# Performance work log

Measured on AMD Instinct MI355X. Metric: run time of the kernel, lower is better.

The kernel has to match this reference:

```python
import jax, jax.numpy as jnp
import numpy as np

B, T, H = 256, 512, 512
NB = 2  # band_names = ['g', 'r']
D_IN = 1 + NB


def setup_inputs() -> dict:
    key = jax.random.key(0)
    ks = jax.random.split(key, 10)
    # serial band assignment: each valid timestep belongs to exactly one band
    band = jax.random.randint(ks[0], (B, T), 0, NB)
    valid = jax.random.uniform(ks[1], (B, T)) < 0.9
    s_onehot = (jax.nn.one_hot(band, NB) * valid[..., None].astype(jnp.float32)).astype(bool)
    onehot = valid
    dtime = jax.random.uniform(ks[2], (B, T))
    encz_last = jax.random.normal(ks[3], (B, H))
    scale = 1.0 / np.sqrt(H).astype(np.float32)
    W_ih = jax.random.normal(ks[4], (3 * H, D_IN)) * scale
    W_hh = jax.random.normal(ks[5], (3 * H, H)) * scale
    b_ih = jax.random.normal(ks[6], (3 * H,)) * scale
    b_hh = jax.random.normal(ks[7], (3 * H,)) * scale
    W1 = jax.random.normal(ks[8], (H, H)) * scale
    b1 = jnp.zeros((H,), jnp.float32)
    W2 = jax.random.normal(ks[9], (1, H)) * scale
    b2 = jnp.zeros((1,), jnp.float32)
    return dict(dtime=dtime, s_onehot=s_onehot, onehot=onehot, encz_last=encz_last,
                W_ih=W_ih, W_hh=W_hh, b_ih=b_ih, b_hh=b_hh, W1=W1, b1=b1, W2=W2, b2=b2)


def gru_masked(x, mask, h0, W_ih, W_hh, b_ih, b_hh):
    """Single-layer GRU (torch gate order r,z,n) with onehot mask: hidden held where mask==False."""
    xp = jnp.einsum('btd,gd->btg', x, W_ih) + b_ih  # [B,T,3H] precomputed input projections

    def step(h, inp):
        xg, m = inp  # xg [B,3H], m [B]
        hg = h @ W_hh.T + b_hh
        xr, xz, xn = jnp.split(xg, 3, axis=-1)
        hr, hz, hn = jnp.split(hg, 3, axis=-1)
        r = jax.nn.sigmoid(xr + hr)
        z = jax.nn.sigmoid(xz + hz)
        n = jnp.tanh(xn + r * hn)
        h_new = (1.0 - z) * n + z * h
        h_out = jnp.where(m[:, None], h_new, h)
        return h_out, h_out

    _, hs = jax.lax.scan(step, h0, (jnp.swapaxes(xp, 0, 1), jnp.swapaxes(mask, 0, 1)))
    return jnp.swapaxes(hs, 0, 1)  # [B,T,H]


def serial_to_parallel(x, m):
    """Compact serial entries where mask m is True to the front of the time axis; zeros elsewhere."""
    pos = jnp.cumsum(m.astype(jnp.int32), axis=1) - 1  # target slot per valid step
    pos = jnp.where(m, pos, 0)
    b_idx = jnp.arange(x.shape[0])[:, None]
    contrib = x * m[..., None].astype(x.dtype)
    return jnp.zeros_like(x).at[b_idx, pos].add(contrib)


def reference(dtime, s_onehot, onehot, encz_last, W_ih, W_hh, b_ih, b_hh, W1, b1, W2, b2):
    decz_in = jnp.concatenate([dtime[..., None], s_onehot.astype(dtime.dtype)], axis=-1)  # [B,T,3]
    decz = gru_masked(decz_in, onehot, encz_last, W_ih, W_hh, b_ih, b_hh)  # [B,T,H]
    hidden = jax.nn.relu(jnp.einsum('bth,oh->bto', decz, W1) + b1)
    decx = jnp.einsum('bth,oh->bto', hidden, W2) + b2  # [B,T,1]
    outs = [serial_to_parallel(decx, s_onehot[..., kb]) for kb in range(s_onehot.shape[-1])]
    return jnp.stack(outs, axis=0)  # [NB,B,T,1] -> model/decx.{b} per band
```

## Files before the change

kernel.cpp:

```cpp
#include <hip/hip_runtime.h>
#include <hip/hip_bf16.h>

#define BB 256
#define TT 512
#define HH 512

typedef float floatx4 __attribute__((ext_vector_type(4)));
typedef short short8 __attribute__((ext_vector_type(8)));

__device__ __forceinline__ unsigned short f2bf(float f) {
    union { float f; unsigned u; } v; v.f = f;
    unsigned r = v.u + 0x7fffu + ((v.u >> 16) & 1u);
    return (unsigned short)(r >> 16);
}
__device__ __forceinline__ float bf2f(unsigned short h) {
    union { unsigned u; float f; } v; v.u = ((unsigned)h) << 16;
    return v.f;
}
__device__ __forceinline__ int frag16(int b, int j) {
    int kin = j & 31;
    return (j >> 5) * 512 + (b + 16 * ((kin >> 2) & 3)) * 8 + ((kin >> 4) << 2) + (kin & 3);
}

__device__ __forceinline__ int ld_sc0(const int* p) {
    int v;
    asm volatile("global_load_dword %0, %1, off sc0\n\ts_waitcnt vmcnt(0)"
                 : "=v"(v) : "v"(p) : "memory");
    return v;
}

__global__ void detect_k(const unsigned char* __restrict__ s, int* __restrict__ flags)
{
    int a = 0, b = 0, c = 0;
    for (int i = blockIdx.x * blockDim.x + threadIdx.x; i < BB * TT * 2;
         i += gridDim.x * blockDim.x) {
        unsigned char v = s[i];
        if (v) {
            int m = i & 3;
            if (m == 1) a = 1;
            else if (m >= 2) b = 1;
            if ((i & 7) == 4) c = 1;
        }
    }
    if (a) atomicOr(flags, 1);
    if (b) atomicOr(flags, 2);
    if (c) atomicOr(flags, 4);
}

__global__ void canon_k(const void* __restrict__ s, const int* __restrict__ flags,
                        unsigned char* __restrict__ canon)
{
    int bt = blockIdx.x * blockDim.x + threadIdx.x;
    if (bt >= BB * TT) return;
    int f = *flags;
    int sg, sr;
    if (f & 1) {
        const unsigned char* p = (const unsigned char*)s;
        sg = p[2 * bt] != 0; sr = p[2 * bt + 1] != 0;
    } else if (f & 2) {
        const float* p = (const float*)s;
        sg = p[2 * bt] != 0.0f; sr = p[2 * bt + 1] != 0.0f;
    } else if (f & 4) {
        const int* p = (const int*)s;
        sg = p[2 * bt] != 0; sr = p[2 * bt + 1] != 0;
    } else {
        const long long* p = (const long long*)s;
        sg = p[2 * bt] != 0; sr = p[2 * bt + 1] != 0;
    }
    canon[bt] = (unsigned char)(sg | (sr << 1));
}

__global__ void h0_k(const float* __restrict__ encz, unsigned* __restrict__ Hp)
{
    int i = blockIdx.x * blockDim.x + threadIdx.x;
    if (i >= BB * HH / 2) return;
    int bg = i >> 8;
    int j  = (i & 255) * 2;
    float f0 = encz[bg * HH + j], f1 = encz[bg * HH + j + 1];
    unsigned short h0b = f2bf(f0), l0b = f2bf(f0 - bf2f(h0b));
    unsigned short h1b = f2bf(f1), l1b = f2bf(f1 - bf2f(h1b));
    int g = bg >> 4, b = bg & 15;
    int fi = frag16(b, j) >> 1;
    unsigned* base = Hp + (size_t)g * 32768;
    base[fi]        = (unsigned)h0b | ((unsigned)h1b << 16);
    base[4096 + fi] = (unsigned)l0b | ((unsigned)l1b << 16);
}

__global__ void w1h_k(const float* __restrict__ W1, unsigned short* __restrict__ W1h)
{
    int idx = blockIdx.x * blockDim.x + threadIdx.x;
    if (idx >= HH * HH) return;
    W1h[idx] = f2bf(W1[idx]);
}

template <bool FAST>
__device__ __forceinline__ void gru_loop(
    unsigned* Hbase, unsigned* hstage,
    const float* dtl, const unsigned char* cnl, float* exch, const float* pwl,
    unsigned short* decz, int* gcs, int* gcf,
    const short8* Bh, const short8* Bl,
    int tid, int w, int l, int wi, int bg0)
{
    int fastspin_en = 1;

    for (int t = 0; t < TT; ++t) {
        const char* src = (const char*)(Hbase + (size_t)(t & 3) * 8192);
        unsigned*   dst = Hbase + (size_t)((t + 1) & 3) * 8192;

        for (int c = w; c < 32; c += 6) {
            const void* gs = src + c * 1024 + l * 16;
            void* ls = (char*)hstage + c * 1024;
            __builtin_amdgcn_global_load_lds(
                (const __attribute__((address_space(1))) unsigned*)gs,
                (__attribute__((address_space(3))) unsigned*)ls, 16, 0,
                FAST ? 0x1 : 0x11);
        }
        __syncthreads();

        floatx4 ac0 = {0.f,0.f,0.f,0.f}, ac1 = {0.f,0.f,0.f,0.f}, ac2 = {0.f,0.f,0.f,0.f};
#pragma unroll
        for (int kt = 0; kt < 16; ++kt) {
            short8 ah = *(const short8*)((const char*)hstage + kt * 1024 + l * 16);
            short8 al = *(const short8*)((const char*)hstage + 16384 + kt * 1024 + l * 16);
            ac0 = __builtin_amdgcn_mfma_f32_16x16x32_bf16(ah, Bh[kt], ac0, 0, 0, 0);
            ac1 = __builtin_amdgcn_mfma_f32_16x16x32_bf16(ah, Bl[kt], ac1, 0, 0, 0);
            ac2 = __builtin_amdgcn_mfma_f32_16x16x32_bf16(al, Bh[kt], ac2, 0, 0, 0);
        }
        floatx4 acc = ac0 + ac1 + ac2;
        *(floatx4*)(exch + w * 256 + l * 4) = acc;
        __syncthreads();

        if (tid < 256) {
            const int b = tid >> 4;
            const int bgl = bg0 + b;
            const float dt = dtl[b * 516 + t];
            const unsigned char cn = cnl[b * 520 + t];
            const float sg = (cn & 1) ? 1.f : 0.f, sr = (cn & 2) ? 1.f : 0.f;
            const int jl0 = (tid * 2) & 31;
            const int j0  = wi * 32 + jl0;
            const int fi  = frag16(b, j0) >> 1;
            const unsigned hiw = hstage[fi];
            const unsigned low = hstage[4096 + fi];
            unsigned short hib[2], lob[2];
#pragma unroll
            for (int p = 0; p < 2; ++p) {
                int jl = jl0 + p;
                int lane16 = (jl & 15) + 16 * (b >> 2);
                int roff = b & 3;
                float a0 = exch[(jl >> 4) * 256 + lane16 * 4 + roff];
                float a1 = exch[(2 + (jl >> 4)) * 256 + lane16 * 4 + roff];
                float a2 = exch[(4 + (jl >> 4)) * 256 + lane16 * 4 + roff];
                float hp = bf2f((unsigned short)(p ? (hiw >> 16) : (hiw & 0xffffu))) +
                           bf2f((unsigned short)(p ? (low >> 16) : (low & 0xffffu)));
                float xr = pwl[0*32+jl]*dt + pwl[1*32+jl]*sg + pwl[2*32+jl]*sr + pwl[9*32+jl];
                float xz = pwl[3*32+jl]*dt + pwl[4*32+jl]*sg + pwl[5*32+jl]*sr + pwl[10*32+jl];
                float xn = pwl[6*32+jl]*dt + pwl[7*32+jl]*sg + pwl[8*32+jl]*sr + pwl[11*32+jl];
                float rr = 1.f / (1.f + __expf(-(xr + a0 + pwl[12*32+jl])));
                float zz = 1.f / (1.f + __expf(-(xz + a1 + pwl[13*32+jl])));
                float tx = xn + rr * (a2 + pwl[14*32+jl]);
                float ex2 = __expf(2.f * fminf(fmaxf(tx, -20.f), 20.f));
                float nn = 1.f - 2.f / (ex2 + 1.f);
                float hnew = (1.f - zz) * nn + zz * hp;
                float ho = cn ? hnew : hp;
                hib[p] = f2bf(ho);
                lob[p] = f2bf(ho - bf2f(hib[p]));
            }
            unsigned hw = (unsigned)hib[0] | ((unsigned)hib[1] << 16);
            unsigned lw = (unsigned)lob[0] | ((unsigned)lob[1] << 16);
            if (FAST) {
                dst[fi] = hw;
                dst[4096 + fi] = lw;
            } else {
                __hip_atomic_store(dst + fi, hw, __ATOMIC_RELAXED, __HIP_MEMORY_SCOPE_AGENT);
                __hip_atomic_store(dst + 4096 + fi, lw, __ATOMIC_RELAXED, __HIP_MEMORY_SCOPE_AGENT);
            }
            ((unsigned*)decz)[(((size_t)bgl * TT + t) * HH + j0) >> 1] = hw;
        }

        if (t != TT - 1) {
            __syncthreads();
            int tgt = (t + 1) * 16;
            if (FAST) {
                if (tid == 64)
                    __hip_atomic_fetch_add(gcs, 1, __ATOMIC_RELAXED,
                                           __HIP_MEMORY_SCOPE_AGENT);
                if (tid == 0) {
                    __hip_atomic_fetch_add(gcf, 1, __ATOMIC_RELAXED,
                                           __HIP_MEMORY_SCOPE_WORKGROUP);
                    int done = 0;
                    if (fastspin_en) {
                        for (int spin = 0; spin < 256; ++spin) {
                            if (ld_sc0(gcf) >= tgt) { done = 1; break; }
                        }
                        if (!done) fastspin_en = 0;
                    }
                    if (!done) {
                        while (__hip_atomic_load(gcs, __ATOMIC_RELAXED,
                                                 __HIP_MEMORY_SCOPE_AGENT) < tgt)
                            __builtin_amdgcn_s_sleep(1);
                    }
                }
            } else {
                if (tid == 0) {
                    __hip_atomic_fetch_add(gcs, 1, __ATOMIC_RELAXED,
                                           __HIP_MEMORY_SCOPE_AGENT);
                    while (__hip_atomic_load(gcs, __ATOMIC_RELAXED,
                                             __HIP_MEMORY_SCOPE_AGENT) < tgt)
                        __builtin_amdgcn_s_sleep(1);
                }
            }
            __syncthreads();
        }
    }
}

__global__ __launch_bounds__(384, 2) void gru_mfma(
    const float* __restrict__ dtime, const unsigned char* __restrict__ canon,
    const float* __restrict__ Wih, const float* __restrict__ Whh,
    const float* __restrict__ bih, const float* __restrict__ bhh,
    unsigned* __restrict__ Hp,
    unsigned short* __restrict__ decz,
    int* __restrict__ sync)
{
    __shared__ __align__(16) unsigned hstage[8192];
    __shared__ float dtl[16 * 516];
    __shared__ unsigned char cnl[16 * 520];
    __shared__ __align__(16) float exch[6 * 256];
    __shared__ float pwl[15 * 32];
    __shared__ int shflag;

    const int g = blockIdx.x & 15, wi = blockIdx.x >> 4;
    const int tid = threadIdx.x, w = tid >> 6, l = tid & 63;
    const int bg0 = g * 16;
    unsigned* Hbase = Hp + (size_t)g * 32768;

    for (int it = tid; it < 16 * 128; it += 384) {
        int b = it >> 7, t4 = it & 127;
        *(float4*)(dtl + b * 516 + t4 * 4) =
            *(const float4*)(dtime + (size_t)(bg0 + b) * TT + t4 * 4);
    }
    for (int it = tid; it < 16 * 128; it += 384) {
        int b = it >> 7, t4 = it & 127;
        *(unsigned*)(cnl + b * 520 + t4 * 4) =
            *(const unsigned*)(canon + (size_t)(bg0 + b) * TT + t4 * 4);
    }
    if (tid < 32) {
        int j = wi * 32 + tid;
        int r1 = HH + j, r2 = 2 * HH + j;
        pwl[0*32+tid] = Wih[j*3];   pwl[1*32+tid] = Wih[j*3+1];  pwl[2*32+tid] = Wih[j*3+2];
        pwl[3*32+tid] = Wih[r1*3];  pwl[4*32+tid] = Wih[r1*3+1]; pwl[5*32+tid] = Wih[r1*3+2];
        pwl[6*32+tid] = Wih[r2*3];  pwl[7*32+tid] = Wih[r2*3+1]; pwl[8*32+tid] = Wih[r2*3+2];
        pwl[9*32+tid]  = bih[j];  pwl[10*32+tid] = bih[r1]; pwl[11*32+tid] = bih[r2];
        pwl[12*32+tid] = bhh[j];  pwl[13*32+tid] = bhh[r1]; pwl[14*32+tid] = bhh[r2];
    }

    const int gate = w >> 1, ch = w & 1;
    const int rB   = gate * HH + wi * 32 + ch * 16 + (l & 15);
    const int kq4  = ((l >> 4) & 3) * 4;
    short8 Bh[16], Bl[16];
#pragma unroll
    for (int kt = 0; kt < 16; ++kt) {
        const float* wp = Whh + (size_t)rB * HH + kt * 32 + kq4;
        float4 f0 = *(const float4*)(wp);
        float4 f1 = *(const float4*)(wp + 16);
        float fs[8] = {f0.x, f0.y, f0.z, f0.w, f1.x, f1.y, f1.z, f1.w};
        short8 bh, bl;
#pragma unroll
        for (int q = 0; q < 8; ++q) {
            unsigned short hb = f2bf(fs[q]);
            bh[q] = (short)hb;
            bl[q] = (short)f2bf(fs[q] - bf2f(hb));
        }
        Bh[kt] = bh; Bl[kt] = bl;
    }

    unsigned xcc;
    asm volatile("s_getreg_b32 %0, hwreg(HW_REG_XCC_ID)" : "=s"(xcc));
    if (tid == 0) {
        __hip_atomic_fetch_or((unsigned*)&sync[1024 + g * 32], 1u << (xcc & 31),
                              __ATOMIC_RELAXED, __HIP_MEMORY_SCOPE_AGENT);
        asm volatile("s_waitcnt vmcnt(0)" ::: "memory");
        __hip_atomic_fetch_add(&sync[1536 + g * 32], 1, __ATOMIC_RELAXED,
                               __HIP_MEMORY_SCOPE_AGENT);
        while (__hip_atomic_load(&sync[1536 + g * 32], __ATOMIC_RELAXED,
                                 __HIP_MEMORY_SCOPE_AGENT) < 16)
            __builtin_amdgcn_s_sleep(2);
        unsigned m = __hip_atomic_load((unsigned*)&sync[1024 + g * 32], __ATOMIC_RELAXED,
                                       __HIP_MEMORY_SCOPE_AGENT);
        shflag = (__popc(m) == 1) ? 1 : 0;
    }
    __syncthreads();
    const int fast = shflag;

    int* gcs = sync + g * 32;
    int* gcf = sync + 512 + g * 32;
    if (fast)
        gru_loop<true>(Hbase, hstage, dtl, cnl, exch, pwl, decz, gcs, gcf, Bh, Bl,
                       tid, w, l, wi, bg0);
    else
        gru_loop<false>(Hbase, hstage, dtl, cnl, exch, pwl, decz, gcs, gcf, Bh, Bl,
                        tid, w, l, wi, bg0);
}

__global__ __launch_bounds__(512) void ff_mfma(
    const unsigned short* __restrict__ decz,
    const unsigned short* __restrict__ W1h,
    const float* __restrict__ b1, const float* __restrict__ W2,
    const float* __restrict__ b2, float* __restrict__ decx)
{
    __shared__ __align__(16) unsigned short wst[512 * 32];

    const int wv = threadIdx.x >> 6, l = threadIdx.x & 63;
    const int row0 = blockIdx.x * 128 + wv * 16;
    const int mrow = l & 15, q = l >> 4;
    const unsigned short* arow = decz + (size_t)(row0 + mrow) * HH;

    floatx4 acc[32];
#pragma unroll
    for (int f = 0; f < 32; ++f) acc[f] = (floatx4){0.f, 0.f, 0.f, 0.f};

    for (int kt = 0; kt < 16; ++kt) {
        __syncthreads();
        for (int it = threadIdx.x; it < 4096; it += 512) {
            int n = it >> 3, q4 = it & 7;
            const unsigned short* gp = W1h + (size_t)n * HH + kt * 32 + q4 * 4;
            uint2 v = *(const uint2*)gp;
            int e0 = (q4 & 3) * 8 + (q4 >> 2) * 4;
            *(uint2*)(wst + n * 32 + e0) = v;
        }
        __syncthreads();

        const int k0 = kt * 32 + q * 4;
        union { unsigned u[4]; short8 s; } a;
        *(uint2*)&a.u[0] = *(const uint2*)(arow + k0);
        *(uint2*)&a.u[2] = *(const uint2*)(arow + k0 + 16);
#pragma unroll
        for (int f = 0; f < 32; ++f) {
            const int n = f * 16 + mrow;
            short8 bh = *(const short8*)(wst + n * 32 + q * 8);
            acc[f] = __builtin_amdgcn_mfma_f32_16x16x32_bf16(a.s, bh, acc[f], 0, 0, 0);
        }
    }

    float res[4] = {0.f, 0.f, 0.f, 0.f};
#pragma unroll
    for (int f = 0; f < 32; ++f) {
        int n = f * 16 + mrow;
        float w2v = W2[n], b1v = b1[n];
#pragma unroll
        for (int i = 0; i < 4; ++i)
            res[i] += w2v * fmaxf(acc[f][i] + b1v, 0.f);
    }
    const float b2v = b2[0];
#pragma unroll
    for (int i = 0; i < 4; ++i) {
        float v = res[i];
        v += __shfl_xor(v, 1, 64);
        v += __shfl_xor(v, 2, 64);
        v += __shfl_xor(v, 4, 64);
        v += __shfl_xor(v, 8, 64);
        if (mrow == 0) decx[row0 + q * 4 + i] = v + b2v;
    }
}

__global__ void scatter_k(const unsigned char* __restrict__ canon,
                          const float* __restrict__ decx, float* __restrict__ out)
{
    int wid = (blockIdx.x * blockDim.x + threadIdx.x) >> 6;
    int lane = threadIdx.x & 63;
    if (wid >= 2 * BB) return;
    int kb = wid >> 8, b = wid & 255;
    int cnt = 0;
    for (int t0 = 0; t0 < TT; t0 += 64) {
        unsigned char c = canon[b * TT + t0 + lane];
        int pred = (c >> kb) & 1;
        unsigned long long m = __ballot(pred);
        if (pred) {
            int pos = cnt + __popcll(m & ((1ull << lane) - 1ull));
            out[((size_t)kb * BB + b) * TT + pos] = decx[b * TT + t0 + lane];
        }
        cnt += __popcll(m);
    }
}

extern "C" void kernel_launch(void* const* d_in, const int* in_sizes, int n_in,
                              void* d_out, int out_size, void* d_ws, size_t ws_size,
                              hipStream_t stream)
{
    const float* dtime    = (const float*)d_in[0];
    const void*  s_onehot = d_in[1];
    const float* encz = (const float*)d_in[3];
    const float* Wih  = (const float*)d_in[4];
    const float* Whh  = (const float*)d_in[5];
    const float* bih  = (const float*)d_in[6];
    const float* bhh  = (const float*)d_in[7];
    const float* W1   = (const float*)d_in[8];
    const float* b1   = (const float*)d_in[9];
    const float* W2   = (const float*)d_in[10];
    const float* b2   = (const float*)d_in[11];

    char* ws = (char*)d_ws;
    int*            sync  = (int*)ws;
    int*            flags = (int*)(ws + 8192);
    unsigned char*  canon = (unsigned char*)(ws + 8704);
    unsigned*       Hp    = (unsigned*)(ws + 8704 + BB * TT);
    unsigned short* decz  = (unsigned short*)((char*)Hp + 16 * 32768 * 4);
    unsigned short* W1h   = (unsigned short*)Hp;
    float*          decx  = (float*)(W1h + HH * HH);

    hipMemsetAsync(ws, 0, 8448, stream);
    detect_k<<<32, 256, 0, stream>>>((const unsigned char*)s_onehot, flags);
    canon_k<<<(BB * TT + 255) / 256, 256, 0, stream>>>(s_onehot, flags, canon);
    h0_k<<<(BB * HH / 2 + 255) / 256, 256, 0, stream>>>(encz, Hp);

    gru_mfma<<<256, 384, 0, stream>>>(dtime, canon, Wih, Whh, bih, bhh,
                                      Hp, decz, sync);

    w1h_k<<<(HH * HH + 255) / 256, 256, 0, stream>>>(W1, W1h);
    ff_mfma<<<BB * TT / 128, 512, 0, stream>>>(decz, W1h, b1, W2, b2, decx);

    hipMemsetAsync(d_out, 0, (size_t)out_size * sizeof(float), stream);
    scatter_k<<<128, 256, 0, stream>>>(canon, decx, (float*)d_out);
}
```

Measured before the change: 1.458 ms.

## Split each GRU block into two independent batch-group streams with LDS spin barriers

Each workgroup now runs two independent 3-wave streams, each handling its own 16-row batch group. Each block covers 16 hidden columns instead of 32, so 32 blocks cooperate per group and grid syncs wait on 32 arrivals. __syncthreads is replaced by per-stream LDS atomic counters, so one stream can compute while the other waits at the inter-block barrier. The per-block dtime and canon LDS preload is dropped in favour of direct global reads each step. The spin loops have iteration caps that break out silently, which could cause incorrect ordering if a wait runs long.

```diff
diff --git a/kernel.cpp b/kernel.cpp
--- a/kernel.cpp
+++ b/kernel.cpp
@@ -79,9 +79,9 @@
     float f0 = encz[bg * HH + j], f1 = encz[bg * HH + j + 1];
     unsigned short h0b = f2bf(f0), l0b = f2bf(f0 - bf2f(h0b));
     unsigned short h1b = f2bf(f1), l1b = f2bf(f1 - bf2f(h1b));
-    int g = bg >> 4, b = bg & 15;
+    int vg = bg >> 4, b = bg & 15;
     int fi = frag16(b, j) >> 1;
-    unsigned* base = Hp + (size_t)g * 32768;
+    unsigned* base = Hp + (size_t)vg * 32768;
     base[fi]        = (unsigned)h0b | ((unsigned)h1b << 16);
     base[4096 + fi] = (unsigned)l0b | ((unsigned)l1b << 16);
 }
@@ -94,70 +94,86 @@
 }
 
 template <bool FAST>
-__device__ __forceinline__ void gru_loop(
-    unsigned* Hbase, unsigned* hstage,
-    const float* dtl, const unsigned char* cnl, float* exch, const float* pwl,
-    unsigned short* decz, int* gcs, int* gcf,
+__device__ __forceinline__ void gru_stream(
+    unsigned* Hb, unsigned* hst, float* exs, const float* pwl,
+    int* arrp, int* gop, int* gcs, int* gcf,
+    const float* dtime, const unsigned char* canon, unsigned short* decz,
     const short8* Bh, const short8* Bl,
-    int tid, int w, int l, int wi, int bg0)
+    int wl, int l, int wi, int vg)
 {
     int fastspin_en = 1;
 
     for (int t = 0; t < TT; ++t) {
-        const char* src = (const char*)(Hbase + (size_t)(t & 3) * 8192);
-        unsigned*   dst = Hbase + (size_t)((t + 1) & 3) * 8192;
-
-        for (int c = w; c < 32; c += 6) {
+        const char* src = (const char*)(Hb + (size_t)(t & 3) * 8192);
+        unsigned*   dst = Hb + (size_t)((t + 1) & 3) * 8192;
+
+        for (int c = wl; c < 32; c += 3) {
             const void* gs = src + c * 1024 + l * 16;
-            void* ls = (char*)hstage + c * 1024;
+            void* ls = (char*)hst + c * 1024;
             __builtin_amdgcn_global_load_lds(
                 (const __attribute__((address_space(1))) unsigned*)gs,
                 (__attribute__((address_space(3))) unsigned*)ls, 16, 0,
                 FAST ? 0x1 : 0x11);
         }
-        __syncthreads();
+        asm volatile("s_waitcnt vmcnt(0)" ::: "memory");
+        {
+            if (l == 0) __hip_atomic_fetch_add(arrp, 1, __ATOMIC_RELEASE,
+                                               __HIP_MEMORY_SCOPE_WORKGROUP);
+            int sp = 0;
+            while (__hip_atomic_load(arrp, __ATOMIC_ACQUIRE,
+                                     __HIP_MEMORY_SCOPE_WORKGROUP) < 9 * t + 3)
+                if (++sp > 40000) break;
+        }
 
         floatx4 ac0 = {0.f,0.f,0.f,0.f}, ac1 = {0.f,0.f,0.f,0.f}, ac2 = {0.f,0.f,0.f,0.f};
 #pragma unroll
         for (int kt = 0; kt < 16; ++kt) {
-            short8 ah = *(const short8*)((const char*)hstage + kt * 1024 + l * 16);
-            short8 al = *(const short8*)((const char*)hstage + 16384 + kt * 1024 + l * 16);
+            short8 ah = *(const short8*)((const char*)hst + kt * 1024 + l * 16);
+            short8 al = *(const short8*)((const char*)hst + 16384 + kt * 1024 + l * 16);
             ac0 = __builtin_amdgcn_mfma_f32_16x16x32_bf16(ah, Bh[kt], ac0, 0, 0, 0);
             ac1 = __builtin_amdgcn_mfma_f32_16x16x32_bf16(ah, Bl[kt], ac1, 0, 0, 0);
             ac2 = __builtin_amdgcn_mfma_f32_16x16x32_bf16(al, Bh[kt], ac2, 0, 0, 0);
         }
         floatx4 acc = ac0 + ac1 + ac2;
-        *(floatx4*)(exch + w * 256 + l * 4) = acc;
-        __syncthreads();
-
-        if (tid < 256) {
-            const int b = tid >> 4;
-            const int bgl = bg0 + b;
-            const float dt = dtl[b * 516 + t];
-            const unsigned char cn = cnl[b * 520 + t];
+        *(floatx4*)(exs + wl * 256 + l * 4) = acc;
+        {
+            if (l == 0) __hip_atomic_fetch_add(arrp, 1, __ATOMIC_RELEASE,
+                                               __HIP_MEMORY_SCOPE_WORKGROUP);
+            int sp = 0;
+            while (__hip_atomic_load(arrp, __ATOMIC_ACQUIRE,
+                                     __HIP_MEMORY_SCOPE_WORKGROUP) < 9 * t + 6)
+                if (++sp > 40000) break;
+        }
+
+        if (wl < 2) {
+            const int ptid = wl * 64 + l;
+            const int pair0 = ptid * 2;
+            const int b = pair0 >> 4, col0 = pair0 & 15;
+            const int bgl = vg * 16 + b;
+            const float dt = dtime[(size_t)bgl * TT + t];
+            const unsigned char cn = canon[(size_t)bgl * TT + t];
             const float sg = (cn & 1) ? 1.f : 0.f, sr = (cn & 2) ? 1.f : 0.f;
-            const int jl0 = (tid * 2) & 31;
-            const int j0  = wi * 32 + jl0;
-            const int fi  = frag16(b, j0) >> 1;
-            const unsigned hiw = hstage[fi];
-            const unsigned low = hstage[4096 + fi];
+            const int j0 = wi * 16 + col0;
+            const int fi = frag16(b, j0) >> 1;
+            const unsigned hiw = hst[fi];
+            const unsigned low = hst[4096 + fi];
             unsigned short hib[2], lob[2];
 #pragma unroll
             for (int p = 0; p < 2; ++p) {
-                int jl = jl0 + p;
-                int lane16 = (jl & 15) + 16 * (b >> 2);
+                int col = col0 + p;
+                int lane16 = col + 16 * (b >> 2);
                 int roff = b & 3;
-                float a0 = exch[(jl >> 4) * 256 + lane16 * 4 + roff];
-                float a1 = exch[(2 + (jl >> 4)) * 256 + lane16 * 4 + roff];
-                float a2 = exch[(4 + (jl >> 4)) * 256 + lane16 * 4 + roff];
+                float a0 = exs[0 * 256 + lane16 * 4 + roff];
+                float a1 = exs[1 * 256 + lane16 * 4 + roff];
+                float a2 = exs[2 * 256 + lane16 * 4 + roff];
                 float hp = bf2f((unsigned short)(p ? (hiw >> 16) : (hiw & 0xffffu))) +
                            bf2f((unsigned short)(p ? (low >> 16) : (low & 0xffffu)));
-                float xr = pwl[0*32+jl]*dt + pwl[1*32+jl]*sg + pwl[2*32+jl]*sr + pwl[9*32+jl];
-                float xz = pwl[3*32+jl]*dt + pwl[4*32+jl]*sg + pwl[5*32+jl]*sr + pwl[10*32+jl];
-                float xn = pwl[6*32+jl]*dt + pwl[7*32+jl]*sg + pwl[8*32+jl]*sr + pwl[11*32+jl];
-                float rr = 1.f / (1.f + __expf(-(xr + a0 + pwl[12*32+jl])));
-                float zz = 1.f / (1.f + __expf(-(xz + a1 + pwl[13*32+jl])));
-                float tx = xn + rr * (a2 + pwl[14*32+jl]);
+                float xr = pwl[0*16+col]*dt + pwl[1*16+col]*sg + pwl[2*16+col]*sr + pwl[9*16+col];
+                float xz = pwl[3*16+col]*dt + pwl[4*16+col]*sg + pwl[5*16+col]*sr + pwl[10*16+col];
+                float xn = pwl[6*16+col]*dt + pwl[7*16+col]*sg + pwl[8*16+col]*sr + pwl[11*16+col];
+                float rr = 1.f / (1.f + __expf(-(xr + a0 + pwl[12*16+col])));
+                float zz = 1.f / (1.f + __expf(-(xz + a1 + pwl[13*16+col])));
+                float tx = xn + rr * (a2 + pwl[14*16+col]);
                 float ex2 = __expf(2.f * fminf(fmaxf(tx, -20.f), 20.f));
                 float nn = 1.f - 2.f / (ex2 + 1.f);
                 float hnew = (1.f - zz) * nn + zz * hp;
@@ -171,45 +187,51 @@
                 dst[fi] = hw;
                 dst[4096 + fi] = lw;
             } else {
-                __hip_atomic_store(dst + fi, hw, __ATOMIC_RELAXED, __HIP_MEMORY_SCOPE_AGENT);
-                __hip_atomic_store(dst + 4096 + fi, lw, __ATOMIC_RELAXED, __HIP_MEMORY_SCOPE_AGENT);
+                __hip_atomic_store(dst + fi, hw, __ATOMIC_RELAXED,
+                                   __HIP_MEMORY_SCOPE_AGENT);
+                __hip_atomic_store(dst + 4096 + fi, lw, __ATOMIC_RELAXED,
+                                   __HIP_MEMORY_SCOPE_AGENT);
             }
             ((unsigned*)decz)[(((size_t)bgl * TT + t) * HH + j0) >> 1] = hw;
         }
+        asm volatile("s_waitcnt vmcnt(0)" ::: "memory");
+        {
+            if (l == 0) __hip_atomic_fetch_add(arrp, 1, __ATOMIC_RELEASE,
+                                               __HIP_MEMORY_SCOPE_WORKGROUP);
+            int sp = 0;
+            while (__hip_atomic_load(arrp, __ATOMIC_ACQUIRE,
+                                     __HIP_MEMORY_SCOPE_WORKGROUP) < 9 * t + 9)
+                if (++sp > 40000) break;
+        }
 
         if (t != TT - 1) {
-            __syncthreads();
-            int tgt = (t + 1) * 16;
-            if (FAST) {
-                if (tid == 64)
-                    __hip_atomic_fetch_add(gcs, 1, __ATOMIC_RELAXED,
-                                           __HIP_MEMORY_SCOPE_AGENT);
-                if (tid == 0) {
+            if (wl == 0 && l == 0) {
+                int tgt = 32 * (t + 1);
+                __hip_atomic_fetch_add(gcs, 1, __ATOMIC_RELAXED,
+                                       __HIP_MEMORY_SCOPE_AGENT);
+                int done = 0;
+                if (FAST) {
                     __hip_atomic_fetch_add(gcf, 1, __ATOMIC_RELAXED,
                                            __HIP_MEMORY_SCOPE_WORKGROUP);
-                    int done = 0;
                     if (fastspin_en) {
                         for (int spin = 0; spin < 256; ++spin) {
                             if (ld_sc0(gcf) >= tgt) { done = 1; break; }
                         }
                         if (!done) fastspin_en = 0;
                     }
-                    if (!done) {
-                        while (__hip_atomic_load(gcs, __ATOMIC_RELAXED,
-                                                 __HIP_MEMORY_SCOPE_AGENT) < tgt)
-                            __builtin_amdgcn_s_sleep(1);
-                    }
                 }
-            } else {
-                if (tid == 0) {
-                    __hip_atomic_fetch_add(gcs, 1, __ATOMIC_RELAXED,
-                                           __HIP_MEMORY_SCOPE_AGENT);
+                if (!done) {
                     while (__hip_atomic_load(gcs, __ATOMIC_RELAXED,
                                              __HIP_MEMORY_SCOPE_AGENT) < tgt)
                         __builtin_amdgcn_s_sleep(1);
                 }
+                __hip_atomic_fetch_add(gop, 1, __ATOMIC_RELEASE,
+                                       __HIP_MEMORY_SCOPE_WORKGROUP);
             }
-            __syncthreads();
+            int sp = 0;
+            while (__hip_atomic_load(gop, __ATOMIC_ACQUIRE,
+                                     __HIP_MEMORY_SCOPE_WORKGROUP) < t + 1)
+                if (++sp > 2000000) break;
         }
     }
 }
@@ -222,41 +244,31 @@
     unsigned short* __restrict__ decz,
     int* __restrict__ sync)
 {
-    __shared__ __align__(16) unsigned hstage[8192];
-    __shared__ float dtl[16 * 516];
-    __shared__ unsigned char cnl[16 * 520];
-    __shared__ __align__(16) float exch[6 * 256];
-    __shared__ float pwl[15 * 32];
+    __shared__ __align__(16) unsigned hstage[2][8192];
+    __shared__ __align__(16) float exch[2][768];
+    __shared__ float pwl[15 * 16];
+    __shared__ int lsync[4];
     __shared__ int shflag;
 
-    const int g = blockIdx.x & 15, wi = blockIdx.x >> 4;
+    const int g = blockIdx.x & 7, wi = blockIdx.x >> 3;
     const int tid = threadIdx.x, w = tid >> 6, l = tid & 63;
-    const int bg0 = g * 16;
-    unsigned* Hbase = Hp + (size_t)g * 32768;
-
-    for (int it = tid; it < 16 * 128; it += 384) {
-        int b = it >> 7, t4 = it & 127;
-        *(float4*)(dtl + b * 516 + t4 * 4) =
-            *(const float4*)(dtime + (size_t)(bg0 + b) * TT + t4 * 4);
-    }
-    for (int it = tid; it < 16 * 128; it += 384) {
-        int b = it >> 7, t4 = it & 127;
-        *(unsigned*)(cnl + b * 520 + t4 * 4) =
-            *(const unsigned*)(canon + (size_t)(bg0 + b) * TT + t4 * 4);
-    }
-    if (tid < 32) {
-        int j = wi * 32 + tid;
+    const int s = (w >= 3) ? 1 : 0, wl = w - 3 * s;
+    const int vg = g * 2 + s;
+    unsigned* Hb = Hp + (size_t)vg * 32768;
+
+    if (tid < 4) lsync[tid] = 0;
+    if (tid < 16) {
+        int j = wi * 16 + tid;
         int r1 = HH + j, r2 = 2 * HH + j;
-        pwl[0*32+tid] = Wih[j*3];   pwl[1*32+tid] = Wih[j*3+1];  pwl[2*32+tid] = Wih[j*3+2];
-        pwl[3*32+tid] = Wih[r1*3];  pwl[4*32+tid] = Wih[r1*3+1]; pwl[5*32+tid] = Wih[r1*3+2];
-        pwl[6*32+tid] = Wih[r2*3];  pwl[7*32+tid] = Wih[r2*3+1]; pwl[8*32+tid] = Wih[r2*3+2];
-        pwl[9*32+tid]  = bih[j];  pwl[10*32+tid] = bih[r1]; pwl[11*32+tid] = bih[r2];
-        pwl[12*32+tid] = bhh[j];  pwl[13*32+tid] = bhh[r1]; pwl[14*32+tid] = bhh[r2];
-    }
-
-    const int gate = w >> 1, ch = w & 1;
-    const int rB   = gate * HH + wi * 32 + ch * 16 + (l & 15);
-    const int kq4  = ((l >> 4) & 3) * 4;
+        pwl[0*16+tid] = Wih[j*3];   pwl[1*16+tid] = Wih[j*3+1];  pwl[2*16+tid] = Wih[j*3+2];
+        pwl[3*16+tid] = Wih[r1*3];  pwl[4*16+tid] = Wih[r1*3+1]; pwl[5*16+tid] = Wih[r1*3+2];
+        pwl[6*16+tid] = Wih[r2*3];  pwl[7*16+tid] = Wih[r2*3+1]; pwl[8*16+tid] = Wih[r2*3+2];
+        pwl[9*16+tid]  = bih[j];  pwl[10*16+tid] = bih[r1]; pwl[11*16+tid] = bih[r2];
+        pwl[12*16+tid] = bhh[j];  pwl[13*16+tid] = bhh[r1]; pwl[14*16+tid] = bhh[r2];
+    }
+
+    const int rB  = wl * HH + wi * 16 + (l & 15);
+    const int kq4 = ((l >> 4) & 3) * 4;
     short8 Bh[16], Bl[16];
 #pragma unroll
     for (int kt = 0; kt < 16; ++kt) {
@@ -283,7 +295,7 @@
         __hip_atomic_fetch_add(&sync[1536 + g * 32], 1, __ATOMIC_RELAXED,
                                __HIP_MEMORY_SCOPE_AGENT);
         while (__hip_atomic_load(&sync[1536 + g * 32], __ATOMIC_RELAXED,
-                                 __HIP_MEMORY_SCOPE_AGENT) < 16)
+                                 __HIP_MEMORY_SCOPE_AGENT) < 32)
             __builtin_amdgcn_s_sleep(2);
         unsigned m = __hip_atomic_load((unsigned*)&sync[1024 + g * 32], __ATOMIC_RELAXED,
                                        __HIP_MEMORY_SCOPE_AGENT);
@@ -292,14 +304,17 @@
     __syncthreads();
     const int fast = shflag;
 
-    int* gcs = sync + g * 32;
-    int* gcf = sync + 512 + g * 32;
+    int* arrp = &lsync[s * 2];
+    int* gop  = &lsync[s * 2 + 1];
+    int* gcs  = sync + vg * 32;
+    int* gcf  = sync + 512 + vg * 32;
+
     if (fast)
-        gru_loop<true>(Hbase, hstage, dtl, cnl, exch, pwl, decz, gcs, gcf, Bh, Bl,
-                       tid, w, l, wi, bg0);
+        gru_stream<true>(Hb, hstage[s], exch[s], pwl, arrp, gop, gcs, gcf,
+                         dtime, canon, decz, Bh, Bl, wl, l, wi, vg);
     else
-        gru_loop<false>(Hbase, hstage, dtl, cnl, exch, pwl, decz, gcs, gcf, Bh, Bl,
-                        tid, w, l, wi, bg0);
+        gru_stream<false>(Hb, hstage[s], exch[s], pwl, arrp, gop, gcs, gcf,
+                          dtime, canon, decz, Bh, Bl, wl, l, wi, vg);
 }
 
 __global__ __launch_bounds__(512) void ff_mfma(
```

New measurement: 2.509 ms. +72.1%, slower.
